# Optimization experiments

Measured on AMD Instinct MI355X. Metric: run time of the kernel, lower is better.

Reference implementation:

```python
import jax, jax.numpy as jnp
import numpy as np

B, T, V, GH, GW = 1, 2, 3, 32, 64
H, W = 224, 448
R = 2                      # splat_radius
RADIUS_SCALE = 1.5
OFFSETS = np.array([(i, j) for i in range(-R, R + 1) for j in range(-R, R + 1)], dtype=np.int32)  # (K,2)


def setup_inputs() -> dict:
    key = jax.random.key(0)
    ks = jax.random.split(key, 9)
    # gaussians roughly in front of the (near-identity) cameras
    xy = jax.random.normal(ks[0], (B, T, V, GH, GW, 2)) * 3.0
    z = jax.random.uniform(ks[1], (B, T, V, GH, GW, 1), minval=1.0, maxval=12.0)
    centers = jnp.concatenate([xy, z], axis=-1)
    scale = jax.random.uniform(ks[2], (B, T, V, GH, GW, 3), minval=0.01, maxval=0.2)
    feat_dc = jax.random.uniform(ks[3], (B, T, V, GH, GW, 3))
    opacity = jax.random.uniform(ks[4], (B, T, V, GH, GW, 1))
    background_prob = jax.random.uniform(ks[5], (B, T, V, GH, GW))
    sem_proj_2d = jax.random.normal(ks[6], (B, T, V, H, W))
    camera_intrinsics = jnp.tile(jnp.array([180.0, 180.0, W / 2.0, H / 2.0]), (B, V, 1))
    eye = jnp.eye(4)
    c2w = jnp.tile(eye, (B, T, V, 1, 1))
    c2w = c2w.at[..., :3, 3].set(jax.random.normal(ks[7], (B, T, V, 3)) * 0.5)
    first_ego_pose_world = jnp.tile(eye, (B, 1, 1))
    return dict(centers=centers, scale=scale, feat_dc=feat_dc, opacity=opacity,
                background_prob=background_prob, sem_proj_2d=sem_proj_2d,
                camera_intrinsics=camera_intrinsics, camera_to_world=c2w,
                first_ego_pose_world=first_ego_pose_world)


def _render_one(world4, scale, color, alpha, intr, w2c):
    # world4: (N,4) homogeneous world points; scale/alpha: (N,); color: (N,3)
    fx, fy, cx, cy = intr[0], intr[1], intr[2], intr[3]
    cam = world4 @ w2c.T                                  # (N,4)
    x, y, z = cam[:, 0], cam[:, 1], cam[:, 2]
    valid = (z > 1e-3) & jnp.all(jnp.isfinite(cam[:, :3]), axis=-1) & (alpha > 1e-5)
    zs = jnp.where(valid, z, 1.0)
    u = jnp.where(valid, x * fx / zs + cx, -1e6)
    v = jnp.where(valid, y * fy / zs + cy, -1e6)
    sigma = jnp.clip((fx + fy) * 0.5 * jnp.abs(scale) / jnp.maximum(zs, 1e-3), 0.75, 10.0)
    inb = (u >= -R - 1.0) & (u <= W + R) & (v >= -R - 1.0) & (v <= H + R)
    valid = valid & inb
    cnt = jnp.sum(valid.astype(jnp.float32))
    sigma_mean = jnp.sum(jnp.where(valid, sigma, 0.0)) / jnp.maximum(cnt, 1.0)
    # depth sort (invalid points pushed to the end, contribute 0)
    order = jnp.argsort(jnp.where(valid, z, jnp.inf))
    u, v, sigma = u[order], v[order], sigma[order]
    alpha_s, color_s, valid_s = alpha[order], color[order], valid[order]
    us = jnp.where(valid_s, u, 0.0)
    vs = jnp.where(valid_s, v, 0.0)
    x0 = jnp.floor(us).astype(jnp.int32)
    y0 = jnp.floor(vs).astype(jnp.int32)
    radii = jnp.clip(jnp.ceil(sigma * RADIUS_SCALE).astype(jnp.int32), 1, R)
    off = jnp.asarray(OFFSETS)                            # (K,2)
    xo = x0[:, None] + off[None, :, 0]                    # (N,K)
    yo = y0[:, None] + off[None, :, 1]
    rkeep = (jnp.abs(off[None, :, 0]) <= radii[:, None]) & (jnp.abs(off[None, :, 1]) <= radii[:, None])
    bkeep = (xo >= 0) & (xo < W) & (yo >= 0) & (yo < H)
    keep = valid_s[:, None] & rkeep & bkeep
    ss = jnp.maximum(sigma, 1e-3)
    du = (us[:, None] - xo.astype(jnp.float32)) / ss[:, None]
    dv = (vs[:, None] - yo.astype(jnp.float32)) / ss[:, None]
    la = jnp.clip(jnp.exp(-0.5 * (du * du + dv * dv)) * alpha_s[:, None], 0.0, 0.999)
    la = jnp.where(keep, la, 0.0)
    idx = jnp.where(keep, yo * W + xo, 0)                 # masked entries add 0 at pixel 0

    def step(carry, inp):
        aden, rgbn = carry
        idx_k, la_k, col_k = inp
        contrib = la_k * jnp.clip(1.0 - aden[idx_k], 0.0, 1.0)   # front-to-back transmittance
        aden = jnp.clip(aden.at[idx_k].add(contrib), 0.0, 0.999)
        rgbn = rgbn.at[:, idx_k].add(col_k[:, None] * contrib[None, :])
        return (aden, rgbn), None

    init = (jnp.zeros(H * W, jnp.float32), jnp.zeros((3, H * W), jnp.float32))
    (aden, rgbn), _ = jax.lax.scan(step, init, (idx, la, color_s))
    touch = jnp.mean((aden > 1e-6).astype(jnp.float32))
    rgb = jnp.clip(rgbn, 0.0, 1.0).reshape(3, H, W)
    return rgb, jnp.clip(aden, 0.0, 1.0).reshape(H, W), sigma_mean, touch


def _render_branch(centers, scales, colors, alpha, intr, c2w, first_pose):
    b, t = centers.shape[0], centers.shape[1]
    v = c2w.shape[2]
    cf = centers.reshape(b, t, -1, 3)
    sf = jnp.mean(scales, axis=-1).reshape(b, t, -1)
    colf = jnp.clip(colors.reshape(b, t, -1, 3), 0.0, 1.0)
    af = jnp.clip(alpha.reshape(b, t, -1), 0.0, 1.0)
    wh = jnp.concatenate([cf, jnp.ones(cf.shape[:-1] + (1,), cf.dtype)], axis=-1)  # (b,t,N,4)
    world = jnp.einsum('bij,btnj->btni', first_pose, wh)
    w2c = jnp.linalg.inv(c2w)                             # (b,t,v,4,4)
    intr_bt = jnp.broadcast_to(intr[:, None], (b, t, v, 4))
    n = cf.shape[2]
    over_views = jax.vmap(_render_one, in_axes=(None, None, None, None, 0, 0))
    over_bt = jax.vmap(over_views, in_axes=(0, 0, 0, 0, 0, 0))
    rgb, ad, sm, tc = over_bt(world.reshape(b * t, n, 4), sf.reshape(b * t, n),
                              colf.reshape(b * t, n, 3), af.reshape(b * t, n),
                              intr_bt.reshape(b * t, v, 4), w2c.reshape(b * t, v, 4, 4))
    rgb = rgb.reshape(b, t, v, 3, H, W)
    ad = ad.reshape(b, t, v, 1, H, W)
    return rgb, ad, jnp.mean(sm), jnp.mean(tc)


def reference(centers, scale, feat_dc, opacity, background_prob, sem_proj_2d,
              camera_intrinsics, camera_to_world, first_ego_pose_world):
    b, t, v, gh, gw = opacity.shape[:5]
    op = jnp.clip(opacity[..., 0], 0.0, 1.0)
    bg = background_prob.reshape(b, t, v, gh, gw)
    dyn = jnp.clip(1.0 - bg, 0.0, 1.0)
    rgb_all, a_all, sm, tr = _render_branch(centers, scale, feat_dc, op,
                                            camera_intrinsics, camera_to_world, first_ego_pose_world)
    rgb_dyn, a_dyn, _, _ = _render_branch(centers, scale, feat_dc, op * dyn,
                                          camera_intrinsics, camera_to_world, first_ego_pose_world)
    rgb_sta, a_sta, _, _ = _render_branch(centers, scale, feat_dc, op * (1.0 - dyn),
                                          camera_intrinsics, camera_to_world, first_ego_pose_world)
    return (rgb_sta, rgb_dyn, rgb_all, a_sta, a_dyn, a_all, sem_proj_2d, sm, tr)
```

## Files before the change

kernel.cpp:

```cpp
#include <hip/hip_runtime.h>
#include <hip/hip_bf16.h>
#include <hip/hip_fp16.h>

namespace {
constexpr int kB = 1, kT = 2, kV = 3;
constexpr int kGH = 32, kGW = 64;
constexpr int kNG = kV * kGH * kGW;
constexpr int kNBT = kB * kT;
constexpr int kNI = kNBT * kV;
constexpr int kH = 224, kW = 448;
constexpr int kHW = kH * kW;

constexpr int kTX = 64, kTY = 4;
constexpr int kTilesX = kW / kTX;
constexpr int kTilesY = kH / kTY;
constexpr int kNTiles = kTilesX * kTilesY;
constexpr int kNBins = kNI * kNTiles;
constexpr int kCAP = 512;
constexpr int kMaxEnt = kNI * kNG;

constexpr size_t RGB_SZ = (size_t)kNI * 3 * kHW;
constexpr size_t A_SZ   = (size_t)kNI * kHW;
constexpr size_t O_RGB_STA = 0;
constexpr size_t O_RGB_DYN = O_RGB_STA + RGB_SZ;
constexpr size_t O_RGB_ALL = O_RGB_DYN + RGB_SZ;
constexpr size_t O_A_STA   = O_RGB_ALL + RGB_SZ;
constexpr size_t O_A_DYN   = O_A_STA + A_SZ;
constexpr size_t O_A_ALL   = O_A_DYN + A_SZ;
constexpr size_t O_SEM     = O_A_ALL + A_SZ;
constexpr size_t O_SM      = O_SEM + A_SZ;
constexpr size_t O_TR      = O_SM + 1;

constexpr size_t WS_W2C   = 128;
constexpr size_t WS_CNTR  = 512;
constexpr size_t WS_TCNT  = 1024;
constexpr size_t WS_TTOUCH= WS_TCNT + (size_t)kNBins * 4;
constexpr size_t WS_TLIST = WS_TTOUCH + (size_t)kNBins * 4;
constexpr size_t WS_PAY   = WS_TLIST + (size_t)kNBins * kCAP * 2;

constexpr int kZeroInts = (int)((WS_TCNT + (size_t)kNBins * 4 - WS_CNTR) / 4);

__device__ __forceinline__ float clip01(float x) { return fminf(fmaxf(x, 0.f), 1.f); }
__device__ __forceinline__ unsigned long long packkey(int zbits, int ikey) {
    return ((unsigned long long)(unsigned)zbits << 32) | (unsigned)ikey;
}
__device__ __forceinline__ float packh2(float a, float b) {
    __half2 h = __floats2half2_rn(a, b);
    return __uint_as_float(*reinterpret_cast<unsigned*>(&h));
}
__device__ __forceinline__ float2 unpackh2(float f) {
    unsigned u = __float_as_uint(f);
    return __half22float2(*reinterpret_cast<__half2*>(&u));
}
}


__global__ __launch_bounds__(256) void k_zero(int* __restrict__ zp,
                                              const float* __restrict__ c2w,
                                              float* __restrict__ w2c) {
    int i = blockIdx.x * 256 + threadIdx.x;
    if (i < kZeroInts) zp[i] = 0;
    if (blockIdx.x == 0 && threadIdx.x < kNI) {
        int inst = threadIdx.x;
        float m[4][8];
        const float* A = c2w + (size_t)inst * 16;
        for (int r = 0; r < 4; ++r)
            for (int cc = 0; cc < 4; ++cc) { m[r][cc] = A[r * 4 + cc]; m[r][cc + 4] = (r == cc) ? 1.f : 0.f; }
        for (int col = 0; col < 4; ++col) {
            int piv = col; float mx = fabsf(m[col][col]);
            for (int r = col + 1; r < 4; ++r) { float a = fabsf(m[r][col]); if (a > mx) { mx = a; piv = r; } }
            if (piv != col)
                for (int cc = 0; cc < 8; ++cc) { float tt = m[col][cc]; m[col][cc] = m[piv][cc]; m[piv][cc] = tt; }
            float inv = 1.f / m[col][col];
            for (int cc = 0; cc < 8; ++cc) m[col][cc] *= inv;
            for (int r = 0; r < 4; ++r) {
                if (r == col) continue;
                float f = m[r][col];
                for (int cc = 0; cc < 8; ++cc) m[r][cc] -= f * m[col][cc];
            }
        }
        for (int r = 0; r < 4; ++r)
            for (int cc = 0; cc < 4; ++cc) w2c[(size_t)inst * 16 + r * 4 + cc] = m[r][cc + 4];
    }
}

__global__ void k_pre(const float* __restrict__ centers, const float* __restrict__ scale,
                      const float* __restrict__ feat, const float* __restrict__ opac,
                      const float* __restrict__ bgp, const float* __restrict__ intr,
                      const float* __restrict__ fpose, const float* __restrict__ w2c,
                      int* __restrict__ entCnt, float* __restrict__ sigmaSum, int* __restrict__ cnt,
                      int* __restrict__ tileCnt, unsigned short* __restrict__ tileList,
                      float* __restrict__ pay) {
    int inst = blockIdx.y;
    int g = blockIdx.x * 256 + threadIdx.x;
    int bt = inst / kV, v = inst % kV;
    int b = bt / kT;

    const float* M = w2c + (size_t)inst * 16;

    const float* c = centers + ((size_t)bt * kNG + g) * 3;
    float c0 = c[0], c1 = c[1], c2 = c[2];
    const float* P = fpose + (size_t)b * 16;
    float wx[4];
#pragma unroll
    for (int i = 0; i < 4; ++i)
        wx[i] = P[i * 4 + 0] * c0 + P[i * 4 + 1] * c1 + P[i * 4 + 2] * c2 + P[i * 4 + 3];

    float camx = M[0] * wx[0] + M[1] * wx[1] + M[2] * wx[2] + M[3] * wx[3];
    float camy = M[4] * wx[0] + M[5] * wx[1] + M[6] * wx[2] + M[7] * wx[3];
    float camz = M[8] * wx[0] + M[9] * wx[1] + M[10] * wx[2] + M[11] * wx[3];

    float op = clip01(opac[(size_t)bt * kNG + g]);
    bool zok = (camz > 0.001f) && isfinite(camx) && isfinite(camy) && isfinite(camz);
    bool valid0 = zok && (op > 1e-5f);

    const float* it = intr + ((size_t)b * kV + v) * 4;
    float fx = it[0], fy = it[1], cx = it[2], cy = it[3];
    float u = camx * fx / camz + cx;
    float vv = camy * fy / camz + cy;

    const float* sp = scale + ((size_t)bt * kNG + g) * 3;
    float sf = (sp[0] + sp[1] + sp[2]) / 3.f;
    float sg = fminf(fmaxf((fx + fy) * 0.5f * fabsf(sf) / fmaxf(camz, 0.001f), 0.75f), 10.f);

    bool inb = (u >= -3.f) && (u <= (float)kW + 2.f) && (vv >= -3.f) && (vv <= (float)kH + 2.f);
    bool statsValid = valid0 && inb;

    float ssum = statsValid ? sg : 0.f;
    int scnt = statsValid ? 1 : 0;
#pragma unroll
    for (int o = 32; o > 0; o >>= 1) {
        ssum += __shfl_down(ssum, o);
        scnt += __shfl_down(scnt, o);
    }
    if ((threadIdx.x & 63) == 0 && scnt > 0) {
        atomicAdd(&sigmaSum[inst], ssum);
        atomicAdd(&cnt[inst], scnt);
    }

    int x0 = (int)floorf(u);
    int y0 = (int)floorf(vv);
    bool emit = statsValid && (x0 >= -2) && (x0 <= kW + 1) && (y0 >= -2) && (y0 <= kH + 1);

    unsigned long long m = __ballot(emit);
    int lane = threadIdx.x & 63;
    int base = 0;
    if (m) {
        int leader = __ffsll((long long)m) - 1;
        if (lane == leader) base = atomicAdd(entCnt, __popcll(m));
        base = __shfl(base, leader);
    }
    if (!emit) return;
    int e = base + __popcll(m & ((1ULL << lane) - 1ULL));

    float bg = bgp[(size_t)bt * kNG + g];
    float dyn = clip01(1.f - bg);
    float aAll = op;
    float aDyn = clip01(op * dyn);
    float aSta = clip01(op * (1.f - dyn));
    if (aDyn <= 1e-5f) aDyn = 0.f;
    if (aSta <= 1e-5f) aSta = 0.f;

    const float* fc = feat + ((size_t)bt * kNG + g) * 3;
    float r = clip01(fc[0]), gc = clip01(fc[1]), bcl = clip01(fc[2]);

    float4* p4 = (float4*)(pay + (size_t)e * 12);
    int keybits = (g << 16) | e;
    p4[0] = make_float4(u, vv, 1.f / fmaxf(sg, 0.001f), aSta);
    p4[1] = make_float4(aDyn, aAll, r, gc);
    p4[2] = make_float4(bcl, camz, __int_as_float(keybits), 0.f);

    int ilo = x0 - 2 < 0 ? 0 : (x0 - 2) / kTX;
    int ihi = min(kTilesX - 1, (x0 + 2) / kTX);
    int jlo = y0 - 2 < 0 ? 0 : (y0 - 2) / kTY;
    int jhi = min(kTilesY - 1, (y0 + 2) / kTY);
    for (int j = jlo; j <= jhi; ++j)
        for (int i = ilo; i <= ihi; ++i) {
            int bin = inst * kNTiles + j * kTilesX + i;
            int idx = atomicAdd(&tileCnt[bin], 1);
            if (idx < kCAP) tileList[(size_t)bin * kCAP + idx] = (unsigned short)e;
        }
}

__global__ __launch_bounds__(256) void k_tile(const int* __restrict__ tileCnt,
                                              const unsigned short* __restrict__ tileList,
                                              const float* __restrict__ pay,
                                              const float* __restrict__ sem,
                                              float* __restrict__ out,
                                              int* __restrict__ tileTouch) {
    __shared__ unsigned long long shKey[kCAP];
    __shared__ float4 shA[kCAP + 8];
    __shared__ float2 shB[kCAP + 8];
    __shared__ int shT[4];

    int t = threadIdx.x;
    int tile = blockIdx.x;
    int inst = blockIdx.y;
    int bin = inst * kNTiles + tile;
    int N = tileCnt[bin];
    if (N > kCAP) N = kCAP;

    unsigned long long kA = ~0ULL, kB = ~0ULL;
    float4 aA, aB; float2 bA, bB;
#define GATHER(i, kq, aq, bq)                                              \
    {   if (i < N) {                                                       \
            int e = tileList[(size_t)bin * kCAP + i];                      \
            const float4* pp = (const float4*)(pay + (size_t)e * 12);      \
            float4 p0 = pp[0], p1 = pp[1], p2 = pp[2];                     \
            kq = packkey(__float_as_int(p2.y), __float_as_int(p2.z));      \
            shKey[i] = kq;                                                 \
            aq = make_float4(p0.x, p0.y, p0.z, packh2(p0.w, p1.x));        \
            bq = make_float2(packh2(p1.y, p1.z), packh2(p1.w, p2.x));      \
        } }
    GATHER(t, kA, aA, bA)
    GATHER(t + 256, kB, aB, bB)
#undef GATHER
    __syncthreads();

    int rA = 0, rB = 0;
    for (int j = 0; j < N; ++j) {
        unsigned long long kj = shKey[j];
        rA += (kj < kA); rB += (kj < kB);
    }
    __syncthreads();
    if (t < N)       { shA[rA] = aA; shB[rA] = bA; }
    if (t + 256 < N) { shA[rB] = aB; shB[rB] = bB; }
    if (t < 8) {
        shA[N + t] = make_float4(0.f, 0.f, 0.f, 0.f);
        shB[N + t] = make_float2(0.f, 0.f);
    }
    __syncthreads();

    int tx = (tile % kTilesX) * kTX;
    int ty = (tile / kTilesX) * kTY;
    int px = tx + (t & (kTX - 1));
    int py = ty + (t >> 6);
    float fpx = (float)px, fpy = (float)py;

    float ad0 = 0.f, ad1 = 0.f, ad2 = 0.f;
    float sr0 = 0.f, sg0 = 0.f, sb0 = 0.f;
    float sr1 = 0.f, sg1 = 0.f, sb1 = 0.f;
    float sr2 = 0.f, sg2 = 0.f, sb2 = 0.f;

    float4 Ac = shA[0]; float2 Bc = shB[0];
    for (int k = 0; k < N; ++k) {
        float4 An = shA[k + 1]; float2 Bn = shB[k + 1];
        float dyc = fpy - floorf(Ac.y);
        if (__any(fabsf(dyc) <= 2.f)) {
            float dxc = fpx - floorf(Ac.x);
            bool keep = (dxc >= -2.f) && (dxc <= 2.f) && (dyc >= -2.f) && (dyc <= 2.f);
            float du = (Ac.x - fpx) * Ac.z;
            float dv = (Ac.y - fpy) * Ac.z;
            float lb = __expf(-0.5f * (du * du + dv * dv));
            lb = keep ? lb : 0.f;
            float2 sd = unpackh2(Ac.w);
            float2 ar = unpackh2(Bc.x);
            float2 gb = unpackh2(Bc.y);
            float la, Tt, ct;
            la = fminf(lb * sd.x, 0.999f);
            Tt = 1.f - ad0; ct = la * Tt;
            ad0 = fminf(ad0 + ct, 0.999f);
            sr0 += ar.y * ct; sg0 += gb.x * ct; sb0 += gb.y * ct;
            la = fminf(lb * sd.y, 0.999f);
            Tt = 1.f - ad1; ct = la * Tt;
            ad1 = fminf(ad1 + ct, 0.999f);
            sr1 += ar.y * ct; sg1 += gb.x * ct; sb1 += gb.y * ct;
            la = fminf(lb * ar.x, 0.999f);
            Tt = 1.f - ad2; ct = la * Tt;
            ad2 = fminf(ad2 + ct, 0.999f);
            sr2 += ar.y * ct; sg2 += gb.x * ct; sb2 += gb.y * ct;
        }
        Ac = An; Bc = Bn;
    }

    unsigned long long tm = __ballot(ad2 > 1e-6f);
    if ((t & 63) == 0) shT[t >> 6] = __popcll(tm);
    __syncthreads();
    if (t == 0) tileTouch[bin] = shT[0] + shT[1] + shT[2] + shT[3];

    size_t o = (size_t)py * kW + px;
    size_t ib3 = (size_t)inst * 3;
    out[O_RGB_STA + (ib3 + 0) * kHW + o] = clip01(sr0);
    out[O_RGB_STA + (ib3 + 1) * kHW + o] = clip01(sg0);
    out[O_RGB_STA + (ib3 + 2) * kHW + o] = clip01(sb0);
    out[O_RGB_DYN + (ib3 + 0) * kHW + o] = clip01(sr1);
    out[O_RGB_DYN + (ib3 + 1) * kHW + o] = clip01(sg1);
    out[O_RGB_DYN + (ib3 + 2) * kHW + o] = clip01(sb1);
    out[O_RGB_ALL + (ib3 + 0) * kHW + o] = clip01(sr2);
    out[O_RGB_ALL + (ib3 + 1) * kHW + o] = clip01(sg2);
    out[O_RGB_ALL + (ib3 + 2) * kHW + o] = clip01(sb2);
    out[O_A_STA + (size_t)inst * kHW + o] = ad0;
    out[O_A_DYN + (size_t)inst * kHW + o] = ad1;
    out[O_A_ALL + (size_t)inst * kHW + o] = ad2;
    out[O_SEM + (size_t)inst * kHW + o] = sem[(size_t)inst * kHW + o];
}

__global__ __launch_bounds__(64) void k_fin(const float* __restrict__ sigmaSum,
                                            const int* __restrict__ cnt,
                                            const int* __restrict__ tileTouch,
                                            float* __restrict__ out) {
    int lane = threadIdx.x;
    float sm = 0.f, tr = 0.f;
    for (int inst = 0; inst < kNI; ++inst) {
        int s = 0;
        for (int i = lane; i < kNTiles; i += 64) s += tileTouch[inst * kNTiles + i];
#pragma unroll
        for (int o = 32; o > 0; o >>= 1) s += __shfl_down(s, o);
        if (lane == 0) {
            sm += sigmaSum[inst] / fmaxf((float)cnt[inst], 1.f);
            tr += (float)s / (float)kHW;
        }
    }
    if (lane == 0) {
        out[O_SM] = sm / (float)kNI;
        out[O_TR] = tr / (float)kNI;
    }
}

extern "C" void kernel_launch(void* const* d_in, const int* in_sizes, int n_in,
                              void* d_out, int out_size, void* d_ws, size_t ws_size,
                              hipStream_t stream) {
    const float* centers = (const float*)d_in[0];
    const float* scal    = (const float*)d_in[1];
    const float* feat    = (const float*)d_in[2];
    const float* opac    = (const float*)d_in[3];
    const float* bgp     = (const float*)d_in[4];
    const float* sem     = (const float*)d_in[5];
    const float* intr    = (const float*)d_in[6];
    const float* c2w     = (const float*)d_in[7];
    const float* fpose   = (const float*)d_in[8];
    float* out = (float*)d_out;
    char* ws = (char*)d_ws;

    float* w2c      = (float*)(ws + WS_W2C);
    int*   entCnt   = (int*)(ws + WS_CNTR);
    float* sigmaSum = (float*)(ws + WS_CNTR + 16);
    int*   cnt      = (int*)(ws + WS_CNTR + 48);
    int*   tileCnt  = (int*)(ws + WS_TCNT);
    int*   tileTouch= (int*)(ws + WS_TTOUCH);
    unsigned short* tileList = (unsigned short*)(ws + WS_TLIST);
    float* pay      = (float*)(ws + WS_PAY);

    k_zero<<<(kZeroInts + 255) / 256, 256, 0, stream>>>((int*)(ws + WS_CNTR), c2w, w2c);

    dim3 gpre(kNG / 256, kNI);
    k_pre<<<gpre, 256, 0, stream>>>(centers, scal, feat, opac, bgp, intr, fpose, w2c,
                                    entCnt, sigmaSum, cnt, tileCnt, tileList, pay);

    dim3 gtile(kNTiles, kNI);
    k_tile<<<gtile, 256, 0, stream>>>(tileCnt, tileList, pay, sem, out, tileTouch);

    k_fin<<<1, 64, 0, stream>>>(sigmaSum, cnt, tileTouch, out);
}
```

Baseline: 73.94 us.

## Remap tile threads to 16x4 wave footprints and stage outputs through shared memory

```diff
diff --git a/kernel.cpp b/kernel.cpp
--- a/kernel.cpp
+++ b/kernel.cpp
@@ -39,6 +39,13 @@
 constexpr size_t WS_PAY   = WS_TLIST + (size_t)kNBins * kCAP * 2;
 
 constexpr int kZeroInts = (int)((WS_TCNT + (size_t)kNBins * 4 - WS_CNTR) / 4);
+
+constexpr int SH_KEY  = 0;
+constexpr int SH_A    = 4096;
+constexpr int SH_B    = 12416;
+constexpr int SH_STG  = 0;
+constexpr int kStgP   = 272;
+constexpr int SH_SIZE = 16576;
 
 __device__ __forceinline__ float clip01(float x) { return fminf(fmaxf(x, 0.f), 1.f); }
 __device__ __forceinline__ unsigned long long packkey(int zbits, int ikey) {
@@ -188,10 +195,12 @@
                                               const float* __restrict__ sem,
                                               float* __restrict__ out,
                                               int* __restrict__ tileTouch) {
-    __shared__ unsigned long long shKey[kCAP];
-    __shared__ float4 shA[kCAP + 8];
-    __shared__ float2 shB[kCAP + 8];
+    __shared__ __align__(16) char smem[SH_SIZE];
     __shared__ int shT[4];
+    unsigned long long* shKey = (unsigned long long*)(smem + SH_KEY);
+    float4* shA = (float4*)(smem + SH_A);
+    float2* shB = (float2*)(smem + SH_B);
+    float*  stage = (float*)(smem + SH_STG);
 
     int t = threadIdx.x;
     int tile = blockIdx.x;
@@ -233,9 +242,10 @@
 
     int tx = (tile % kTilesX) * kTX;
     int ty = (tile / kTilesX) * kTY;
-    int px = tx + (t & (kTX - 1));
-    int py = ty + (t >> 6);
-    float fpx = (float)px, fpy = (float)py;
+    int wv = t >> 6, lane = t & 63;
+    int clx = wv * 16 + (lane & 15);
+    int cly = lane >> 4;
+    float fpx = (float)(tx + clx), fpy = (float)(ty + cly);
 
     float ad0 = 0.f, ad1 = 0.f, ad2 = 0.f;
     float sr0 = 0.f, sg0 = 0.f, sb0 = 0.f;
@@ -245,10 +255,10 @@
     float4 Ac = shA[0]; float2 Bc = shB[0];
     for (int k = 0; k < N; ++k) {
         float4 An = shA[k + 1]; float2 Bn = shB[k + 1];
+        float dxc = fpx - floorf(Ac.x);
         float dyc = fpy - floorf(Ac.y);
-        if (__any(fabsf(dyc) <= 2.f)) {
-            float dxc = fpx - floorf(Ac.x);
-            bool keep = (dxc >= -2.f) && (dxc <= 2.f) && (dyc >= -2.f) && (dyc <= 2.f);
+        bool keep = (dxc >= -2.f) && (dxc <= 2.f) && (dyc >= -2.f) && (dyc <= 2.f);
+        if (__any(keep)) {
             float du = (Ac.x - fpx) * Ac.z;
             float dv = (Ac.y - fpy) * Ac.z;
             float lb = __expf(-0.5f * (du * du + dv * dv));
@@ -275,23 +285,40 @@
 
     unsigned long long tm = __ballot(ad2 > 1e-6f);
     if ((t & 63) == 0) shT[t >> 6] = __popcll(tm);
-    __syncthreads();
+
+    __syncthreads();
+    int ci = cly * 68 + clx;
+    stage[0 * kStgP + ci] = clip01(sr0);
+    stage[1 * kStgP + ci] = clip01(sg0);
+    stage[2 * kStgP + ci] = clip01(sb0);
+    stage[3 * kStgP + ci] = clip01(sr1);
+    stage[4 * kStgP + ci] = clip01(sg1);
+    stage[5 * kStgP + ci] = clip01(sb1);
+    stage[6 * kStgP + ci] = clip01(sr2);
+    stage[7 * kStgP + ci] = clip01(sg2);
+    stage[8 * kStgP + ci] = clip01(sb2);
+    stage[9 * kStgP + ci] = ad0;
+    stage[10 * kStgP + ci] = ad1;
+    stage[11 * kStgP + ci] = ad2;
+    __syncthreads();
+
     if (t == 0) tileTouch[bin] = shT[0] + shT[1] + shT[2] + shT[3];
 
-    size_t o = (size_t)py * kW + px;
+    int si = (t >> 6) * 68 + (t & 63);
+    size_t o = (size_t)(ty + (t >> 6)) * kW + tx + (t & 63);
     size_t ib3 = (size_t)inst * 3;
-    out[O_RGB_STA + (ib3 + 0) * kHW + o] = clip01(sr0);
-    out[O_RGB_STA + (ib3 + 1) * kHW + o] = clip01(sg0);
-    out[O_RGB_STA + (ib3 + 2) * kHW + o] = clip01(sb0);
-    out[O_RGB_DYN + (ib3 + 0) * kHW + o] = clip01(sr1);
-    out[O_RGB_DYN + (ib3 + 1) * kHW + o] = clip01(sg1);
-    out[O_RGB_DYN + (ib3 + 2) * kHW + o] = clip01(sb1);
-    out[O_RGB_ALL + (ib3 + 0) * kHW + o] = clip01(sr2);
-    out[O_RGB_ALL + (ib3 + 1) * kHW + o] = clip01(sg2);
-    out[O_RGB_ALL + (ib3 + 2) * kHW + o] = clip01(sb2);
-    out[O_A_STA + (size_t)inst * kHW + o] = ad0;
-    out[O_A_DYN + (size_t)inst * kHW + o] = ad1;
-    out[O_A_ALL + (size_t)inst * kHW + o] = ad2;
+    out[O_RGB_STA + (ib3 + 0) * kHW + o] = stage[0 * kStgP + si];
+    out[O_RGB_STA + (ib3 + 1) * kHW + o] = stage[1 * kStgP + si];
+    out[O_RGB_STA + (ib3 + 2) * kHW + o] = stage[2 * kStgP + si];
+    out[O_RGB_DYN + (ib3 + 0) * kHW + o] = stage[3 * kStgP + si];
+    out[O_RGB_DYN + (ib3 + 1) * kHW + o] = stage[4 * kStgP + si];
+    out[O_RGB_DYN + (ib3 + 2) * kHW + o] = stage[5 * kStgP + si];
+    out[O_RGB_ALL + (ib3 + 0) * kHW + o] = stage[6 * kStgP + si];
+    out[O_RGB_ALL + (ib3 + 1) * kHW + o] = stage[7 * kStgP + si];
+    out[O_RGB_ALL + (ib3 + 2) * kHW + o] = stage[8 * kStgP + si];
+    out[O_A_STA + (size_t)inst * kHW + o] = stage[9 * kStgP + si];
+    out[O_A_DYN + (size_t)inst * kHW + o] = stage[10 * kStgP + si];
+    out[O_A_ALL + (size_t)inst * kHW + o] = stage[11 * kStgP + si];
     out[O_SEM + (size_t)inst * kHW + o] = sem[(size_t)inst * kHW + o];
 }
 
```

Result: faster. 68.91 us (-6.8%).
